# Kernel optimization log

Hardware: AMD Instinct MI355X
Metric: run time of the kernel (lower is better)

## Reference

```python
import jax, jax.numpy as jnp
import numpy as np

B, N, E, H = 8, 512, 256, 8
HD = E // H
FF = 4 * E
TOPK = max(1, int(N * 0.2))
FW_MAX_DIST = 10      # default of get_shortest_path_matrix
EMB_MAX_IDX = 6       # spd encoder: max_dist(5) + 1
LN_EPS = 1e-5


def _layernorm(x, g, b):
    m = jnp.mean(x, axis=-1, keepdims=True)
    v = jnp.var(x, axis=-1, keepdims=True)
    return (x - m) / jnp.sqrt(v + LN_EPS) * g + b


def setup_inputs() -> dict:
    key = jax.random.key(0)
    ks = jax.random.split(key, 12)
    s = 0.02
    return {
        "x": jax.random.normal(ks[0], (B, N, E), jnp.float32),
        "adj": jax.random.uniform(ks[1], (B, N, N), jnp.float32),
        "emb_spd": (jax.random.normal(ks[2], (EMB_MAX_IDX + 1, H), jnp.float32) * s),
        "w_qkv": jax.random.normal(ks[3], (3 * E, E), jnp.float32) * s,
        "b_qkv": jnp.zeros((3 * E,), jnp.float32),
        "w_out": jax.random.normal(ks[4], (E, E), jnp.float32) * s,
        "b_out": jnp.zeros((E,), jnp.float32),
        "w_ff1": jax.random.normal(ks[5], (FF, E), jnp.float32) * s,
        "b_ff1": jnp.zeros((FF,), jnp.float32),
        "w_ff2": jax.random.normal(ks[6], (E, FF), jnp.float32) * s,
        "b_ff2": jnp.zeros((E,), jnp.float32),
        "g1": jnp.ones((E,), jnp.float32),
        "beta1": jnp.zeros((E,), jnp.float32),
        "g2": jnp.ones((E,), jnp.float32),
        "beta2": jnp.zeros((E,), jnp.float32),
        "w_pool": jax.random.normal(ks[7], (1, E), jnp.float32) * s,
        "b_pool": jnp.zeros((1,), jnp.float32),
    }


def _combined_mask(adj, emb_spd):
    # top-k per row -> binary adjacency via scatter
    _, idx = jax.lax.top_k(adj, TOPK)                       # [B,N,k]
    bi = jnp.arange(B)[:, None, None]
    ri = jnp.arange(N)[None, :, None]
    binary = jnp.zeros_like(adj).at[bi, ri, idx].set(1.0)   # [B,N,N]

    # Floyd-Warshall shortest paths
    dist = jnp.where(binary == 1.0, 1.0, jnp.inf)
    ids = jnp.arange(N)
    dist = dist.at[:, ids, ids].set(0.0)

    def body(k, d):
        return jnp.minimum(d, d[:, :, k][:, :, None] + d[:, k, :][:, None, :])

    dist = jax.lax.fori_loop(0, N, body, dist)
    dist_i = jnp.where(dist > FW_MAX_DIST, -1.0, dist).astype(jnp.int32)

    # spatial bias embedding: indices = clamp(dist+1, 0, max_dist+1)
    sp_idx = jnp.clip(dist_i + 1, 0, EMB_MAX_IDX)           # [B,N,N]
    bias = jnp.transpose(emb_spd[sp_idx], (0, 3, 1, 2))     # [B,H,N,N]

    base = jnp.where(binary == 0.0, -jnp.inf, 0.0)[:, None] # [B,1,N,N]
    return base + bias                                      # [B,H,N,N]


def reference(x, adj, emb_spd, w_qkv, b_qkv, w_out, b_out,
              w_ff1, b_ff1, w_ff2, b_ff2, g1, beta1, g2, beta2,
              w_pool, b_pool):
    mask = _combined_mask(adj, emb_spd)                     # [B,H,N,N]

    # multi-head self-attention (PyTorch MHA, post-norm encoder layer, eval)
    qkv = x @ w_qkv.T + b_qkv                               # [B,N,3E]
    q, k, v = jnp.split(qkv, 3, axis=-1)
    q = q.reshape(B, N, H, HD).transpose(0, 2, 1, 3)
    k = k.reshape(B, N, H, HD).transpose(0, 2, 1, 3)
    v = v.reshape(B, N, H, HD).transpose(0, 2, 1, 3)
    scores = jnp.einsum("bhqd,bhkd->bhqk", q, k) / np.sqrt(HD) + mask
    attn = jax.nn.softmax(scores, axis=-1)
    ctx = jnp.einsum("bhqk,bhkd->bhqd", attn, v)
    ctx = ctx.transpose(0, 2, 1, 3).reshape(B, N, E)
    attn_out = ctx @ w_out.T + b_out

    x1 = _layernorm(x + attn_out, g1, beta1)
    ff = jax.nn.relu(x1 @ w_ff1.T + b_ff1) @ w_ff2.T + b_ff2
    x2 = _layernorm(x1 + ff, g2, beta2)

    # attention pooling over nodes
    w = jax.nn.softmax(jnp.tanh(x2 @ w_pool.T + b_pool), axis=1)  # [B,N,1]
    return jnp.sum(x2 * w, axis=1)                          # [B,E]
```

## Files before the change

### kernel.cpp

```cpp
#include <hip/hip_runtime.h>
#include <math.h>


#define B_ 8
#define N_ 512
#define E_ 256
#define H_ 8
#define HD_ 32
#define TOPK_ 102

typedef __attribute__((ext_vector_type(8))) short bf16x8;
typedef __attribute__((ext_vector_type(4))) float f32x4;

__device__ __forceinline__ unsigned short f2b(float f) {
  unsigned u = __builtin_bit_cast(unsigned, f);
  return (unsigned short)((u + 0x7FFFu + ((u >> 16) & 1u)) >> 16);
}

__global__ __launch_bounds__(256) void cvt_topk(
    const float* __restrict__ adj, unsigned int* __restrict__ bits,
    const float* __restrict__ x, const float* __restrict__ wqkv,
    const float* __restrict__ wout, const float* __restrict__ wff1,
    const float* __restrict__ wff2, unsigned short* __restrict__ xb,
    unsigned short* __restrict__ wqkvb, unsigned short* __restrict__ woutb,
    unsigned short* __restrict__ wff1b, unsigned short* __restrict__ wff2b) {
  __shared__ unsigned int hist[1024];
  __shared__ float cval[64];
  __shared__ int cidx[64];
  __shared__ int s_cnt, s_bb, s_need;
  __shared__ unsigned int rowbits[16];
  __shared__ int wsum[4];
  const int t = threadIdx.x;

  if (blockIdx.x >= 4096) {
    int i = ((blockIdx.x - 4096) * 256 + t) * 4;
    const float* src;
    unsigned short* dst;
    int off;
    if (i < 1048576)      { src = x;    dst = xb;    off = i; }
    else if (i < 1245184) { src = wqkv; dst = wqkvb; off = i - 1048576; }
    else if (i < 1310720) { src = wout; dst = woutb; off = i - 1245184; }
    else if (i < 1572864) { src = wff1; dst = wff1b; off = i - 1310720; }
    else                  { src = wff2; dst = wff2b; off = i - 1572864; }
    float4 v = *(const float4*)(src + off);
    ushort4 o;
    o.x = f2b(v.x); o.y = f2b(v.y); o.z = f2b(v.z); o.w = f2b(v.w);
    *(ushort4*)(dst + off) = o;
    return;
  }
  const int row = blockIdx.x;
  const float* a = adj + (size_t)row * N_;
  const int lane = t & 63;
  const int wave = t >> 6;

  hist[t] = 0u; hist[t + 256] = 0u; hist[t + 512] = 0u; hist[t + 768] = 0u;
  if (t == 0) s_cnt = 0;
  float v0 = a[t];
  float v1 = a[t + 256];
  __syncthreads();
  const int b0 = min(1023, max(0, (int)(v0 * 1024.0f)));
  const int b1 = min(1023, max(0, (int)(v1 * 1024.0f)));
  atomicAdd(&hist[b0], 1u);
  atomicAdd(&hist[b1], 1u);
  __syncthreads();
  const int base = 1020 - 4 * t;
  const int h0 = (int)hist[base], h1 = (int)hist[base + 1];
  const int h2 = (int)hist[base + 2], h3 = (int)hist[base + 3];
  const int g = h0 + h1 + h2 + h3;
  int sc = g;
  #pragma unroll
  for (int off = 1; off < 64; off <<= 1) {
    int y = __shfl_up(sc, off);
    sc += (lane >= off) ? y : 0;
  }
  if (lane == 63) wsum[wave] = sc;
  __syncthreads();
  int wo = 0;
  for (int w = 0; w < wave; w++) wo += wsum[w];
  const int incl = sc + wo;
  const int excl = incl - g;
  if (excl < TOPK_ && incl >= TOPK_) {
    int cum = excl;
    int bb = base;
    const int hh[4] = {h3, h2, h1, h0};
    const int bs[4] = {base + 3, base + 2, base + 1, base};
    #pragma unroll
    for (int u = 0; u < 4; u++) {
      if (cum + hh[u] >= TOPK_) { bb = bs[u]; break; }
      cum += hh[u];
    }
    s_bb = bb;
    s_need = TOPK_ - cum;
  }
  __syncthreads();
  const int bb = s_bb;
  const int need = s_need;
  const bool sel0 = (b0 > bb);
  const bool sel1 = (b1 > bb);
  if (b0 == bb) { int p = atomicAdd(&s_cnt, 1); if (p < 64) { cval[p] = v0; cidx[p] = t; } }
  if (b1 == bb) { int p = atomicAdd(&s_cnt, 1); if (p < 64) { cval[p] = v1; cidx[p] = t + 256; } }
  unsigned long long m0 = __ballot(sel0);
  unsigned long long m1 = __ballot(sel1);
  if (lane == 0) {
    rowbits[2 * wave + 0] = (unsigned int)m0;
    rowbits[2 * wave + 1] = (unsigned int)(m0 >> 32);
    rowbits[8 + 2 * wave + 0] = (unsigned int)m1;
    rowbits[8 + 2 * wave + 1] = (unsigned int)(m1 >> 32);
  }
  __syncthreads();
  const int cnt = min(s_cnt, 64);
  for (int c = t; c < cnt; c += 256) {
    const float v = cval[c];
    const int idx = cidx[c];
    int r = 0;
    for (int j = 0; j < cnt; j++) {
      const float vj = cval[j];
      const int ij = cidx[j];
      if (vj > v || (vj == v && ij < idx)) r++;
    }
    if (r < need) atomicOr(&rowbits[idx >> 5], 1u << (idx & 31));
  }
  __syncthreads();
  if (t < 16) bits[(size_t)row * 16 + t] = rowbits[t];
}

__global__ __launch_bounds__(256) void gemm_mfma(
    const unsigned short* __restrict__ A, const unsigned short* __restrict__ W,
    const float* __restrict__ bias, const float* __restrict__ res,
    void* __restrict__ Cout, unsigned short* __restrict__ kG,
    unsigned short* __restrict__ vG, int M, int N, int K, int flags) {
  __shared__ __align__(16) unsigned short Af[8 * 64 * 8];
  __shared__ __align__(16) unsigned short Wf[8 * 64 * 8];
  const int tid = threadIdx.x;
  const int m0 = blockIdx.y * 64, n0 = blockIdx.x * 64;
  const int wave = tid >> 6, lane = tid & 63;
  const int wm = wave & 1, wn = wave >> 1;
  const int q = lane >> 4, l15 = lane & 15;
  const int r = tid >> 2, c0 = tid & 3;

  f32x4 acc[2][2];
  #pragma unroll
  for (int i = 0; i < 2; i++)
    #pragma unroll
    for (int j = 0; j < 2; j++) acc[i][j] = (f32x4){0.f, 0.f, 0.f, 0.f};

  const size_t arow = (size_t)(m0 + r) * K;
  const size_t wrow = (size_t)(n0 + r) * K;
  for (int k0 = 0; k0 < K; k0 += 64) {
    uint4 a0 = *(const uint4*)(A + arow + k0 + c0 * 8);
    uint4 a1 = *(const uint4*)(A + arow + k0 + (c0 + 4) * 8);
    uint4 w0 = *(const uint4*)(W + wrow + k0 + c0 * 8);
    uint4 w1 = *(const uint4*)(W + wrow + k0 + (c0 + 4) * 8);
    __syncthreads();
    {
      int kc = c0 >> 2, qq = c0 & 3;
      int s0 = ((r >> 4) * 2 + kc) * 64 + (r & 15) + qq * 16;
      int kc1 = (c0 + 4) >> 2, qq1 = (c0 + 4) & 3;
      int s1 = ((r >> 4) * 2 + kc1) * 64 + (r & 15) + qq1 * 16;
      *(uint4*)(Af + s0 * 8) = a0;
      *(uint4*)(Af + s1 * 8) = a1;
      *(uint4*)(Wf + s0 * 8) = w0;
      *(uint4*)(Wf + s1 * 8) = w1;
    }
    __syncthreads();
    #pragma unroll
    for (int kc = 0; kc < 2; kc++) {
      bf16x8 af[2], wf[2];
      #pragma unroll
      for (int mt = 0; mt < 2; mt++)
        af[mt] = *(const bf16x8*)(Af + (((wm * 2 + mt) * 2 + kc) * 64 + lane) * 8);
      #pragma unroll
      for (int nt = 0; nt < 2; nt++)
        wf[nt] = *(const bf16x8*)(Wf + (((wn * 2 + nt) * 2 + kc) * 64 + lane) * 8);
      #pragma unroll
      for (int mt = 0; mt < 2; mt++)
        #pragma unroll
        for (int nt = 0; nt < 2; nt++)
          acc[mt][nt] = __builtin_amdgcn_mfma_f32_16x16x32_bf16(af[mt], wf[nt], acc[mt][nt], 0, 0, 0);
    }
  }
  #pragma unroll
  for (int nt = 0; nt < 2; nt++) {
    const int col = n0 + (wn * 2 + nt) * 16 + l15;
    const float bv = bias[col];
    #pragma unroll
    for (int mt = 0; mt < 2; mt++) {
      const int rowb = m0 + (wm * 2 + mt) * 16 + q * 4;
      float ov[4];
      #pragma unroll
      for (int reg = 0; reg < 4; reg++) {
        float o = acc[mt][nt][reg] + bv;
        if (res) o += res[(size_t)(rowb + reg) * N + col];
        if (flags & 1) o = fmaxf(o, 0.f);
        ov[reg] = o;
      }
      if (flags & 4) {
        if (col < 256) {
          #pragma unroll
          for (int reg = 0; reg < 4; reg++)
            ((unsigned short*)Cout)[(size_t)(rowb + reg) * 256 + col] = f2b(ov[reg]);
        } else if (col < 512) {
          const int dfull = col - 256;
          const int hh2 = dfull >> 5, d = dfull & 31;
          const int q2 = d >> 3, sub = d & 7;
          const int bidx = rowb >> 9, j = rowb & 511;
          const int jt = j >> 6, jtile = (j >> 4) & 3, jl = j & 15;
          unsigned short* kp = kG +
              ((size_t)(((bidx * 8 + hh2) * 8 + jt) * 4 + jtile) * 64 + q2 * 16 + jl) * 8 + sub;
          kp[0] = f2b(ov[0]); kp[8] = f2b(ov[1]); kp[16] = f2b(ov[2]); kp[24] = f2b(ov[3]);
        } else {
          const int dfull = col - 512;
          const int hh2 = dfull >> 5, d = dfull & 31;
          const int dt = d >> 4, dl = d & 15;
          const int bidx = rowb >> 9, j = rowb & 511;
          const int jt = j >> 6, jj = j & 63;
          const int kc = jj >> 5, q2 = (jj >> 3) & 3, sub0 = jj & 7;
          ushort4 st;
          st.x = f2b(ov[0]); st.y = f2b(ov[1]); st.z = f2b(ov[2]); st.w = f2b(ov[3]);
          *(ushort4*)(vG +
              ((size_t)(((bidx * 8 + hh2) * 8 + jt) * 4 + dt * 2 + kc) * 64 + q2 * 16 + dl) * 8 + sub0) = st;
        }
      } else if (flags & 2) {
        #pragma unroll
        for (int reg = 0; reg < 4; reg++)
          ((unsigned short*)Cout)[(size_t)(rowb + reg) * N + col] = f2b(ov[reg]);
      } else {
        #pragma unroll
        for (int reg = 0; reg < 4; reg++)
          ((float*)Cout)[(size_t)(rowb + reg) * N + col] = ov[reg];
      }
    }
  }
}

__global__ __launch_bounds__(256) void attn_mfma(
    const unsigned short* __restrict__ qb, const unsigned short* __restrict__ kG,
    const unsigned short* __restrict__ vG, const unsigned int* __restrict__ bits,
    const float* __restrict__ emb, unsigned short* __restrict__ ctxo) {
  const int bx = blockIdx.x;
  const int ib = bx & 7;
  const int h = (bx >> 3) & 7;
  const int b = bx >> 6;
  const int tid = threadIdx.x;
  const int lane = tid & 63;
  const int wave = tid >> 6;
  const int q = lane >> 4, l15 = lane & 15;

  __shared__ __align__(16) unsigned int mrow[64 * 16];
  __shared__ __align__(16) unsigned short pF[4][2 * 64 * 8];

  {
    int rr = tid >> 2, wq = tid & 3;
    uint4 mw = *(const uint4*)(bits + ((size_t)(b * N_ + ib * 64 + rr)) * 16 + wq * 4);
    *(uint4*)(mrow + rr * 16 + wq * 4) = mw;
  }
  __syncthreads();

  const int i0w = ib * 64 + wave * 16;
  const bf16x8 qf = *(const bf16x8*)(qb + ((size_t)(b * N_ + i0w + l15)) * 256 + h * HD_ + q * 8);
  const float delta = emb[1 * H_ + h] - emb[2 * H_ + h];
  const float scale = 0.17677669529663687f;

  float m_run[4], l_run[4];
  #pragma unroll
  for (int e = 0; e < 4; e++) { m_run[e] = -1e30f; l_run[e] = 0.f; }
  f32x4 cacc[2];
  cacc[0] = (f32x4){0.f, 0.f, 0.f, 0.f};
  cacc[1] = (f32x4){0.f, 0.f, 0.f, 0.f};

  unsigned short* pbase = &pF[wave][0];
  const unsigned short* kb = kG + (size_t)(b * 8 + h) * 8 * 4 * 512;
  const unsigned short* vb = vG + (size_t)(b * 8 + h) * 8 * 4 * 512;

  #pragma unroll 1
  for (int jt = 0; jt < 8; jt++) {
    f32x4 s4[4];
    #pragma unroll
    for (int jtile = 0; jtile < 4; jtile++) {
      bf16x8 kf = *(const bf16x8*)(kb + (size_t)(jt * 4 + jtile) * 512 + lane * 8);
      s4[jtile] = __builtin_amdgcn_mfma_f32_16x16x32_bf16(qf, kf, (f32x4){0.f, 0.f, 0.f, 0.f}, 0, 0, 0);
    }
    unsigned long long mw64[4];
    #pragma unroll
    for (int reg = 0; reg < 4; reg++)
      mw64[reg] = *(const unsigned long long*)(mrow + (wave * 16 + q * 4 + reg) * 16 + jt * 2);
    float smat[4][4];
    #pragma unroll
    for (int jtile = 0; jtile < 4; jtile++) {
      #pragma unroll
      for (int reg = 0; reg < 4; reg++) {
        unsigned int w = (jtile & 2) ? (unsigned int)(mw64[reg] >> 32) : (unsigned int)mw64[reg];
        bool allowed = ((w >> ((jtile & 1) * 16 + l15)) & 1u) != 0u;
        int ig = ib * 64 + wave * 16 + q * 4 + reg;
        int jg = jt * 64 + jtile * 16 + l15;
        float s = s4[jtile][reg] * scale + ((jg == ig) ? delta : 0.f);
        smat[jtile][reg] = allowed ? s : -INFINITY;
      }
    }
    float alpha[4], pmat[4][4];
    #pragma unroll
    for (int reg = 0; reg < 4; reg++) {
      float mloc = fmaxf(fmaxf(smat[0][reg], smat[1][reg]), fmaxf(smat[2][reg], smat[3][reg]));
      #pragma unroll
      for (int off = 1; off < 16; off <<= 1) mloc = fmaxf(mloc, __shfl_xor(mloc, off));
      float mnew = fmaxf(m_run[reg], mloc);
      alpha[reg] = __expf(m_run[reg] - mnew);
      m_run[reg] = mnew;
      float ps = 0.f;
      #pragma unroll
      for (int jtile = 0; jtile < 4; jtile++) {
        float p = __expf(smat[jtile][reg] - mnew);
        pmat[jtile][reg] = p;
        ps += p;
      }
      #pragma unroll
      for (int off = 1; off < 16; off <<= 1) ps += __shfl_xor(ps, off);
      l_run[reg] = l_run[reg] * alpha[reg] + ps;
      cacc[0][reg] *= alpha[reg];
      cacc[1][reg] *= alpha[reg];
    }
    #pragma unroll
    for (int jtile = 0; jtile < 4; jtile++) {
      int j_l = jtile * 16 + l15;
      int sl = ((j_l >> 5) * 64 + ((j_l >> 3) & 3) * 16) * 8 + (j_l & 7);
      #pragma unroll
      for (int reg = 0; reg < 4; reg++)
        pbase[sl + (q * 4 + reg) * 8] = f2b(pmat[jtile][reg]);
    }
    #pragma unroll
    for (int kc = 0; kc < 2; kc++) {
      bf16x8 pf = *(const bf16x8*)(pbase + (kc * 64 + lane) * 8);
      #pragma unroll
      for (int dt = 0; dt < 2; dt++) {
        bf16x8 vf = *(const bf16x8*)(vb + (size_t)(jt * 4 + dt * 2 + kc) * 512 + lane * 8);
        cacc[dt] = __builtin_amdgcn_mfma_f32_16x16x32_bf16(pf, vf, cacc[dt], 0, 0, 0);
      }
    }
  }
  #pragma unroll
  for (int reg = 0; reg < 4; reg++) {
    const float linv = 1.f / l_run[reg];
    const size_t row = (size_t)(b * N_ + i0w + q * 4 + reg);
    #pragma unroll
    for (int dt = 0; dt < 2; dt++)
      ctxo[row * E_ + h * HD_ + dt * 16 + l15] = f2b(cacc[dt][reg] * linv);
  }
}

__global__ __launch_bounds__(256) void ln8_kernel(
    const float* __restrict__ t, const float* __restrict__ g,
    const float* __restrict__ be, float* __restrict__ out,
    unsigned short* __restrict__ outb) {
  __shared__ float sh[8];
  const int tid = threadIdx.x;
  const int wave = tid >> 6, lane = tid & 63;
  const float gv = g[tid], bev = be[tid];
  #pragma unroll 1
  for (int rr = 0; rr < 8; rr++) {
    const int row = blockIdx.x * 8 + rr;
    float v = t[(size_t)row * E_ + tid];
    float s = v, s2 = v * v;
    #pragma unroll
    for (int off = 32; off > 0; off >>= 1) {
      s += __shfl_xor(s, off);
      s2 += __shfl_xor(s2, off);
    }
    __syncthreads();
    if (lane == 0) { sh[wave] = s; sh[4 + wave] = s2; }
    __syncthreads();
    s = sh[0] + sh[1] + sh[2] + sh[3];
    s2 = sh[4] + sh[5] + sh[6] + sh[7];
    float mean = s * (1.f / 256.f);
    float var = s2 * (1.f / 256.f) - mean * mean;
    float inv = rsqrtf(var + 1e-5f);
    float o = (v - mean) * inv * gv + bev;
    out[(size_t)row * E_ + tid] = o;
    outb[(size_t)row * E_ + tid] = f2b(o);
  }
}

__global__ __launch_bounds__(256) void ln2pool_kernel(
    const float* __restrict__ t, const float* __restrict__ g,
    const float* __restrict__ be, const float* __restrict__ wp,
    const float* __restrict__ bp, float* __restrict__ partial,
    float* __restrict__ pwsum) {
  __shared__ float sh[8];
  const int tid = threadIdx.x;
  const int wave = tid >> 6, lane = tid & 63;
  const int c = blockIdx.x;
  const float gv = g[tid], bev = be[tid], wpv = wp[tid], bpv = bp[0];
  float pacc = 0.f, esum = 0.f;
  #pragma unroll 1
  for (int rr = 0; rr < 8; rr++) {
    const int row = c * 8 + rr;
    float v = t[(size_t)row * E_ + tid];
    float s = v, s2 = v * v;
    #pragma unroll
    for (int off = 32; off > 0; off >>= 1) {
      s += __shfl_xor(s, off);
      s2 += __shfl_xor(s2, off);
    }
    __syncthreads();
    if (lane == 0) { sh[wave] = s; sh[4 + wave] = s2; }
    __syncthreads();
    s = sh[0] + sh[1] + sh[2] + sh[3];
    s2 = sh[4] + sh[5] + sh[6] + sh[7];
    float mean = s * (1.f / 256.f);
    float var = s2 * (1.f / 256.f) - mean * mean;
    float inv = rsqrtf(var + 1e-5f);
    float o = (v - mean) * inv * gv + bev;
    float d = o * wpv;
    #pragma unroll
    for (int off = 32; off > 0; off >>= 1) d += __shfl_xor(d, off);
    __syncthreads();
    if (lane == 0) sh[wave] = d;
    __syncthreads();
    float dot = sh[0] + sh[1] + sh[2] + sh[3] + bpv;
    float e = __expf(tanhf(dot));
    pacc += e * o;
    esum += e;
  }
  partial[(size_t)c * E_ + tid] = pacc;
  if (tid == 0) pwsum[c] = esum;
}

__global__ __launch_bounds__(256) void pool_final(
    const float* __restrict__ partial, const float* __restrict__ pwsum,
    float* __restrict__ out) {
  const int b = blockIdx.x;
  const int tid = threadIdx.x;
  float acc = 0.f, ws = 0.f;
  #pragma unroll
  for (int c = 0; c < 64; c++) acc += partial[(size_t)(b * 64 + c) * E_ + tid];
  #pragma unroll
  for (int c = 0; c < 64; c++) ws += pwsum[b * 64 + c];
  out[b * E_ + tid] = acc / ws;
}

extern "C" void kernel_launch(void* const* d_in, const int* in_sizes, int n_in,
                              void* d_out, int out_size, void* d_ws, size_t ws_size,
                              hipStream_t stream) {
  (void)in_sizes; (void)n_in; (void)out_size; (void)ws_size;
  const float* x      = (const float*)d_in[0];
  const float* adj    = (const float*)d_in[1];
  const float* emb    = (const float*)d_in[2];
  const float* w_qkv  = (const float*)d_in[3];
  const float* b_qkv  = (const float*)d_in[4];
  const float* w_out  = (const float*)d_in[5];
  const float* b_out  = (const float*)d_in[6];
  const float* w_ff1  = (const float*)d_in[7];
  const float* b_ff1  = (const float*)d_in[8];
  const float* w_ff2  = (const float*)d_in[9];
  const float* b_ff2  = (const float*)d_in[10];
  const float* g1     = (const float*)d_in[11];
  const float* be1    = (const float*)d_in[12];
  const float* g2     = (const float*)d_in[13];
  const float* be2    = (const float*)d_in[14];
  const float* w_pool = (const float*)d_in[15];
  const float* b_pool = (const float*)d_in[16];

  char* ws = (char*)d_ws;
  unsigned int*   bits  = (unsigned int*)ws;
  unsigned short* xb    = (unsigned short*)(ws + 262144);
  unsigned short* qb    = (unsigned short*)(ws + 2359296);
  unsigned short* kG    = (unsigned short*)(ws + 4456448);
  unsigned short* vG    = (unsigned short*)(ws + 6553600);
  unsigned short* ctxb  = (unsigned short*)(ws + 8650752);
  float*          tbuf  = (float*)(ws + 10747904);
  float*          x1    = (float*)(ws + 14942208);
  unsigned short* x1b   = (unsigned short*)(ws + 19136512);
  unsigned short* hffb  = (unsigned short*)(ws + 21233664);
  unsigned short* wqkvb = (unsigned short*)(ws + 29622272);
  unsigned short* woutb = (unsigned short*)(ws + 30015488);
  unsigned short* wff1b = (unsigned short*)(ws + 30146560);
  unsigned short* wff2b = (unsigned short*)(ws + 30670848);
  float*          partial = (float*)(ws + 31195136);
  float*          pwsum   = (float*)(ws + 31719424);
  float*          outp  = (float*)d_out;

  const int M = B_ * N_;

  cvt_topk<<<4096 + 1792, 256, 0, stream>>>(adj, bits, x, w_qkv, w_out, w_ff1,
                                            w_ff2, xb, wqkvb, woutb, wff1b, wff2b);
  gemm_mfma<<<dim3(768 / 64, M / 64), 256, 0, stream>>>(
      xb, wqkvb, b_qkv, nullptr, qb, kG, vG, M, 768, E_, 4);
  attn_mfma<<<B_ * H_ * (N_ / 64), 256, 0, stream>>>(qb, kG, vG, bits, emb, ctxb);
  gemm_mfma<<<dim3(E_ / 64, M / 64), 256, 0, stream>>>(
      ctxb, woutb, b_out, x, tbuf, nullptr, nullptr, M, E_, E_, 0);
  ln8_kernel<<<M / 8, 256, 0, stream>>>(tbuf, g1, be1, x1, x1b);
  gemm_mfma<<<dim3(1024 / 64, M / 64), 256, 0, stream>>>(
      x1b, wff1b, b_ff1, nullptr, hffb, nullptr, nullptr, M, 1024, E_, 1 | 2);
  gemm_mfma<<<dim3(E_ / 64, M / 64), 256, 0, stream>>>(
      hffb, wff2b, b_ff2, x1, tbuf, nullptr, nullptr, M, E_, 1024, 0);
  ln2pool_kernel<<<M / 8, 256, 0, stream>>>(tbuf, g2, be2, w_pool, b_pool,
                                            partial, pwsum);
  pool_final<<<B_, 256, 0, stream>>>(partial, pwsum, outp);
}
```

Baseline: 178.5 us.

## Fuse LayerNorm1 into out-proj epilogue stats and FF GEMM prologues

Removes the standalone LayerNorm1 kernel. The out-projection GEMM now accumulates per-row sum and sum-of-squares with atomics into a stats buffer, which the conversion kernel zeroes. FF1 applies the normalization on the fly while loading its fp32 A operand, and FF2 re-normalizes the residual in its epilogue. This saves a launch and the x1/x1b round trip, at the cost of fp32 A loads in FF1, redundant normalization math, and atomic contention on row stats.

After: 175.5 us. No clear change (-1.6%).

```diff
diff --git a/kernel.cpp b/kernel.cpp
--- a/kernel.cpp
+++ b/kernel.cpp
@@ -17,13 +17,37 @@
   return (unsigned short)((u + 0x7FFFu + ((u >> 16) & 1u)) >> 16);
 }
 
+__device__ __forceinline__ uint4 lnpack(const float* __restrict__ p,
+                                        const float* __restrict__ g,
+                                        const float* __restrict__ b,
+                                        float mean, float inv) {
+  float4 v0 = *(const float4*)p, v1 = *(const float4*)(p + 4);
+  float4 g0 = *(const float4*)g, g1 = *(const float4*)(g + 4);
+  float4 b0 = *(const float4*)b, b1 = *(const float4*)(b + 4);
+  unsigned short h0 = f2b((v0.x - mean) * inv * g0.x + b0.x);
+  unsigned short h1 = f2b((v0.y - mean) * inv * g0.y + b0.y);
+  unsigned short h2 = f2b((v0.z - mean) * inv * g0.z + b0.z);
+  unsigned short h3 = f2b((v0.w - mean) * inv * g0.w + b0.w);
+  unsigned short h4 = f2b((v1.x - mean) * inv * g1.x + b1.x);
+  unsigned short h5 = f2b((v1.y - mean) * inv * g1.y + b1.y);
+  unsigned short h6 = f2b((v1.z - mean) * inv * g1.z + b1.z);
+  unsigned short h7 = f2b((v1.w - mean) * inv * g1.w + b1.w);
+  uint4 u;
+  u.x = (unsigned)h0 | ((unsigned)h1 << 16);
+  u.y = (unsigned)h2 | ((unsigned)h3 << 16);
+  u.z = (unsigned)h4 | ((unsigned)h5 << 16);
+  u.w = (unsigned)h6 | ((unsigned)h7 << 16);
+  return u;
+}
+
 __global__ __launch_bounds__(256) void cvt_topk(
     const float* __restrict__ adj, unsigned int* __restrict__ bits,
     const float* __restrict__ x, const float* __restrict__ wqkv,
     const float* __restrict__ wout, const float* __restrict__ wff1,
     const float* __restrict__ wff2, unsigned short* __restrict__ xb,
     unsigned short* __restrict__ wqkvb, unsigned short* __restrict__ woutb,
-    unsigned short* __restrict__ wff1b, unsigned short* __restrict__ wff2b) {
+    unsigned short* __restrict__ wff1b, unsigned short* __restrict__ wff2b,
+    float* __restrict__ rstat) {
   __shared__ unsigned int hist[1024];
   __shared__ float cval[64];
   __shared__ int cidx[64];
@@ -32,6 +56,11 @@
   __shared__ int wsum[4];
   const int t = threadIdx.x;
 
+  if (blockIdx.x >= 5888) {
+    int i4 = (blockIdx.x - 5888) * 1024 + t * 4;
+    *(float4*)(rstat + i4) = (float4){0.f, 0.f, 0.f, 0.f};
+    return;
+  }
   if (blockIdx.x >= 4096) {
     int i = ((blockIdx.x - 4096) * 256 + t) * 4;
     const float* src;
@@ -124,11 +153,14 @@
   if (t < 16) bits[(size_t)row * 16 + t] = rowbits[t];
 }
 
+template <int FLAGS>
 __global__ __launch_bounds__(256) void gemm_mfma(
-    const unsigned short* __restrict__ A, const unsigned short* __restrict__ W,
-    const float* __restrict__ bias, const float* __restrict__ res,
-    void* __restrict__ Cout, unsigned short* __restrict__ kG,
-    unsigned short* __restrict__ vG, int M, int N, int K, int flags) {
+    const unsigned short* __restrict__ A, const float* __restrict__ A32,
+    const unsigned short* __restrict__ W, const float* __restrict__ bias,
+    const float* __restrict__ res, void* __restrict__ Cout,
+    unsigned short* __restrict__ kG, unsigned short* __restrict__ vG,
+    float* __restrict__ rstat, const float* __restrict__ lng,
+    const float* __restrict__ lnb, int M, int N, int K) {
   __shared__ __align__(16) unsigned short Af[8 * 64 * 8];
   __shared__ __align__(16) unsigned short Wf[8 * 64 * 8];
   const int tid = threadIdx.x;
@@ -144,11 +176,28 @@
     #pragma unroll
     for (int j = 0; j < 2; j++) acc[i][j] = (f32x4){0.f, 0.f, 0.f, 0.f};
 
+  float lmean = 0.f, linv = 0.f;
+  if (FLAGS & 16) {
+    float s = rstat[(size_t)(m0 + r) * 2];
+    float s2 = rstat[(size_t)(m0 + r) * 2 + 1];
+    lmean = s * (1.f / 256.f);
+    float var = s2 * (1.f / 256.f) - lmean * lmean;
+    linv = rsqrtf(var + 1e-5f);
+  }
+
   const size_t arow = (size_t)(m0 + r) * K;
   const size_t wrow = (size_t)(n0 + r) * K;
   for (int k0 = 0; k0 < K; k0 += 64) {
-    uint4 a0 = *(const uint4*)(A + arow + k0 + c0 * 8);
-    uint4 a1 = *(const uint4*)(A + arow + k0 + (c0 + 4) * 8);
+    uint4 a0, a1;
+    if (FLAGS & 16) {
+      a0 = lnpack(A32 + arow + k0 + c0 * 8, lng + k0 + c0 * 8,
+                  lnb + k0 + c0 * 8, lmean, linv);
+      a1 = lnpack(A32 + arow + k0 + (c0 + 4) * 8, lng + k0 + (c0 + 4) * 8,
+                  lnb + k0 + (c0 + 4) * 8, lmean, linv);
+    } else {
+      a0 = *(const uint4*)(A + arow + k0 + c0 * 8);
+      a1 = *(const uint4*)(A + arow + k0 + (c0 + 4) * 8);
+    }
     uint4 w0 = *(const uint4*)(W + wrow + k0 + c0 * 8);
     uint4 w1 = *(const uint4*)(W + wrow + k0 + (c0 + 4) * 8);
     __syncthreads();
@@ -179,6 +228,13 @@
           acc[mt][nt] = __builtin_amdgcn_mfma_f32_16x16x32_bf16(af[mt], wf[nt], acc[mt][nt], 0, 0, 0);
     }
   }
+  float srow[2][4], sqrow[2][4];
+  if (FLAGS & 8) {
+    #pragma unroll
+    for (int mt = 0; mt < 2; mt++)
+      #pragma unroll
+      for (int reg = 0; reg < 4; reg++) { srow[mt][reg] = 0.f; sqrow[mt][reg] = 0.f; }
+  }
   #pragma unroll
   for (int nt = 0; nt < 2; nt++) {
     const int col = n0 + (wn * 2 + nt) * 16 + l15;
@@ -190,11 +246,24 @@
       #pragma unroll
       for (int reg = 0; reg < 4; reg++) {
         float o = acc[mt][nt][reg] + bv;
-        if (res) o += res[(size_t)(rowb + reg) * N + col];
-        if (flags & 1) o = fmaxf(o, 0.f);
+        if (res) {
+          float rv = res[(size_t)(rowb + reg) * N + col];
+          if (FLAGS & 32) {
+            const int rr = rowb + reg;
+            float s = rstat[(size_t)rr * 2];
+            float s2 = rstat[(size_t)rr * 2 + 1];
+            float mn = s * (1.f / 256.f);
+            float vv = s2 * (1.f / 256.f) - mn * mn;
+            float iv = rsqrtf(vv + 1e-5f);
+            rv = (rv - mn) * iv * lng[col] + lnb[col];
+          }
+          o += rv;
+        }
+        if (FLAGS & 1) o = fmaxf(o, 0.f);
+        if (FLAGS & 8) { srow[mt][reg] += o; sqrow[mt][reg] += o * o; }
         ov[reg] = o;
       }
-      if (flags & 4) {
+      if (FLAGS & 4) {
         if (col < 256) {
           #pragma unroll
           for (int reg = 0; reg < 4; reg++)
@@ -220,7 +289,7 @@
           *(ushort4*)(vG +
               ((size_t)(((bidx * 8 + hh2) * 8 + jt) * 4 + dt * 2 + kc) * 64 + q2 * 16 + dl) * 8 + sub0) = st;
         }
-      } else if (flags & 2) {
+      } else if (FLAGS & 2) {
         #pragma unroll
         for (int reg = 0; reg < 4; reg++)
           ((unsigned short*)Cout)[(size_t)(rowb + reg) * N + col] = f2b(ov[reg]);
@@ -230,6 +299,24 @@
           ((float*)Cout)[(size_t)(rowb + reg) * N + col] = ov[reg];
       }
     }
+  }
+  if (FLAGS & 8) {
+    #pragma unroll
+    for (int mt = 0; mt < 2; mt++)
+      #pragma unroll
+      for (int reg = 0; reg < 4; reg++) {
+        float s = srow[mt][reg], s2 = sqrow[mt][reg];
+        #pragma unroll
+        for (int off = 1; off < 16; off <<= 1) {
+          s += __shfl_xor(s, off);
+          s2 += __shfl_xor(s2, off);
+        }
+        if (l15 == 0) {
+          const int row = m0 + (wm * 2 + mt) * 16 + q * 4 + reg;
+          atomicAdd(&rstat[(size_t)row * 2], s);
+          atomicAdd(&rstat[(size_t)row * 2 + 1], s2);
+        }
+      }
   }
 }
 
@@ -344,38 +431,6 @@
     #pragma unroll
     for (int dt = 0; dt < 2; dt++)
       ctxo[row * E_ + h * HD_ + dt * 16 + l15] = f2b(cacc[dt][reg] * linv);
-  }
-}
-
-__global__ __launch_bounds__(256) void ln8_kernel(
-    const float* __restrict__ t, const float* __restrict__ g,
-    const float* __restrict__ be, float* __restrict__ out,
-    unsigned short* __restrict__ outb) {
-  __shared__ float sh[8];
-  const int tid = threadIdx.x;
-  const int wave = tid >> 6, lane = tid & 63;
-  const float gv = g[tid], bev = be[tid];
-  #pragma unroll 1
-  for (int rr = 0; rr < 8; rr++) {
-    const int row = blockIdx.x * 8 + rr;
-    float v = t[(size_t)row * E_ + tid];
-    float s = v, s2 = v * v;
-    #pragma unroll
-    for (int off = 32; off > 0; off >>= 1) {
-      s += __shfl_xor(s, off);
-      s2 += __shfl_xor(s2, off);
-    }
-    __syncthreads();
-    if (lane == 0) { sh[wave] = s; sh[4 + wave] = s2; }
-    __syncthreads();
-    s = sh[0] + sh[1] + sh[2] + sh[3];
-    s2 = sh[4] + sh[5] + sh[6] + sh[7];
-    float mean = s * (1.f / 256.f);
-    float var = s2 * (1.f / 256.f) - mean * mean;
-    float inv = rsqrtf(var + 1e-5f);
-    float o = (v - mean) * inv * gv + bev;
-    out[(size_t)row * E_ + tid] = o;
-    outb[(size_t)row * E_ + tid] = f2b(o);
   }
 }
 
@@ -467,8 +522,8 @@
   unsigned short* vG    = (unsigned short*)(ws + 6553600);
   unsigned short* ctxb  = (unsigned short*)(ws + 8650752);
   float*          tbuf  = (float*)(ws + 10747904);
-  float*          x1    = (float*)(ws + 14942208);
-  unsigned short* x1b   = (unsigned short*)(ws + 19136512);
+  float*          tbuf2 = (float*)(ws + 14942208);
+  float*          rstat = (float*)(ws + 19136512);
   unsigned short* hffb  = (unsigned short*)(ws + 21233664);
   unsigned short* wqkvb = (unsigned short*)(ws + 29622272);
   unsigned short* woutb = (unsigned short*)(ws + 30015488);
@@ -480,19 +535,23 @@
 
   const int M = B_ * N_;
 
-  cvt_topk<<<4096 + 1792, 256, 0, stream>>>(adj, bits, x, w_qkv, w_out, w_ff1,
-                                            w_ff2, xb, wqkvb, woutb, wff1b, wff2b);
-  gemm_mfma<<<dim3(768 / 64, M / 64), 256, 0, stream>>>(
-      xb, wqkvb, b_qkv, nullptr, qb, kG, vG, M, 768, E_, 4);
+  cvt_topk<<<4096 + 1792 + 2, 256, 0, stream>>>(
+      adj, bits, x, w_qkv, w_out, w_ff1, w_ff2, xb, wqkvb, woutb, wff1b,
+      wff2b, rstat);
+  gemm_mfma<4><<<dim3(768 / 64, M / 64), 256, 0, stream>>>(
+      xb, nullptr, wqkvb, b_qkv, nullptr, qb, kG, vG, nullptr, nullptr,
+      nullptr, M, 768, E_);
   attn_mfma<<<B_ * H_ * (N_ / 64), 256, 0, stream>>>(qb, kG, vG, bits, emb, ctxb);
-  gemm_mfma<<<dim3(E_ / 64, M / 64), 256, 0, stream>>>(
-      ctxb, woutb, b_out, x, tbuf, nullptr, nullptr, M, E_, E_, 0);
-  ln8_kernel<<<M / 8, 256, 0, stream>>>(tbuf, g1, be1, x1, x1b);
-  gemm_mfma<<<dim3(1024 / 64, M / 64), 256, 0, stream>>>(
-      x1b, wff1b, b_ff1, nullptr, hffb, nullptr, nullptr, M, 1024, E_, 1 | 2);
-  gemm_mfma<<<dim3(E_ / 64, M / 64), 256, 0, stream>>>(
-      hffb, wff2b, b_ff2, x1, tbuf, nullptr, nullptr, M, E_, 1024, 0);
-  ln2pool_kernel<<<M / 8, 256, 0, stream>>>(tbuf, g2, be2, w_pool, b_pool,
+  gemm_mfma<8><<<dim3(E_ / 64, M / 64), 256, 0, stream>>>(
+      ctxb, nullptr, woutb, b_out, x, tbuf, nullptr, nullptr, rstat, nullptr,
+      nullptr, M, E_, E_);
+  gemm_mfma<1 | 2 | 16><<<dim3(1024 / 64, M / 64), 256, 0, stream>>>(
+      nullptr, tbuf, wff1b, b_ff1, nullptr, hffb, nullptr, nullptr, rstat,
+      g1, be1, M, 1024, E_);
+  gemm_mfma<32><<<dim3(E_ / 64, M / 64), 256, 0, stream>>>(
+      hffb, nullptr, wff2b, b_ff2, tbuf, tbuf2, nullptr, nullptr, rstat,
+      g1, be1, M, E_, 1024);
+  ln2pool_kernel<<<M / 8, 256, 0, stream>>>(tbuf2, g2, be2, w_pool, b_pool,
                                             partial, pwsum);
   pool_final<<<B_, 256, 0, stream>>>(partial, pwsum, outp);
 }
```
